# Kernel tuning notes

Measured on AMD Instinct MI355X. Metric: run time of the kernel, lower is better.

The kernel has to match this reference:

```python
import jax, jax.numpy as jnp
import numpy as np

N = 100000      # nodes per node type
E = 500000      # edges per relation
DIN = 128
DOUT = 128
H = 8
DK = DOUT // H  # 16
SQRT_DK = float(np.sqrt(DK))


def setup_inputs() -> dict:
    key = jax.random.key(0)
    ks = jax.random.split(key, 24)
    s = 1.0 / np.sqrt(DIN)
    inp = {
        "h_a": jax.random.normal(ks[0], (N, DIN), jnp.float32),
        "h_b": jax.random.normal(ks[1], (N, DIN), jnp.float32),
        "src0": jax.random.randint(ks[2], (E,), 0, N, jnp.int32),
        "dst0": jax.random.randint(ks[3], (E,), 0, N, jnp.int32),
        "src1": jax.random.randint(ks[4], (E,), 0, N, jnp.int32),
        "dst1": jax.random.randint(ks[5], (E,), 0, N, jnp.int32),
        "src2": jax.random.randint(ks[6], (E,), 0, N, jnp.int32),
        "dst2": jax.random.randint(ks[7], (E,), 0, N, jnp.int32),
        "Wk": jax.random.normal(ks[8], (2, DIN, DOUT), jnp.float32) * s,
        "bk": jnp.zeros((2, DOUT), jnp.float32),
        "Wv": jax.random.normal(ks[9], (2, DIN, DOUT), jnp.float32) * s,
        "bv": jnp.zeros((2, DOUT), jnp.float32),
        "Wq": jax.random.normal(ks[10], (2, DIN, DOUT), jnp.float32) * s,
        "bq": jnp.zeros((2, DOUT), jnp.float32),
        "Wa": jax.random.normal(ks[11], (2, DOUT, DOUT), jnp.float32) * s,
        "ba": jnp.zeros((2, DOUT), jnp.float32),
        # xavier_uniform-like scale for [H, DK, DK] relation transforms
        "rel_att": jax.random.normal(ks[12], (3, H, DK, DK), jnp.float32) * (1.0 / np.sqrt(DK)),
        "rel_msg": jax.random.normal(ks[13], (3, H, DK, DK), jnp.float32) * (1.0 / np.sqrt(DK)),
        "rel_pri": 1.0 + 0.1 * jax.random.normal(ks[14], (3, H), jnp.float32),
        "skip": jnp.zeros((2,), jnp.float32),
    }
    return inp


def _relation(x_src, x_dst, src, dst, Wk_, bk_, Wv_, bv_, Wq_, bq_, att, msg, pri):
    """One canonical edge type: returns scatter-sum aggregation t [N, H, DK]."""
    k = (x_src @ Wk_ + bk_).reshape(-1, H, DK)
    k = jnp.einsum('nhd,hde->nhe', k, att)                     # relation-specific key transform
    v = jnp.einsum('nhd,hde->nhe', (x_src @ Wv_ + bv_).reshape(-1, H, DK), msg)
    q = (x_dst @ Wq_ + bq_).reshape(-1, H, DK)
    # per-edge dot-product score [E, H] (v_dot_u with q on dst, k on src)
    score = jnp.einsum('ehd,ehd->eh', q[dst], k[src]) * pri / SQRT_DK
    # edge softmax grouped by dst node
    smax = jax.ops.segment_max(score, dst, num_segments=N)
    smax = jnp.where(jnp.isfinite(smax), smax, 0.0)            # empty dst groups
    ex = jnp.exp(score - smax[dst])
    den = jax.ops.segment_sum(ex, dst, num_segments=N)
    a = ex / den[dst]                                          # [E, H]
    # message = v[src] * a, scatter-sum to dst
    return jax.ops.segment_sum(v[src] * a[..., None], dst, num_segments=N)


def reference(h_a, h_b, src0, dst0, src1, dst1, src2, dst2,
              Wk, bk, Wv, bv, Wq, bq, Wa, ba,
              rel_att, rel_msg, rel_pri, skip):
    # relations: 0: a->b, 1: b->a, 2: a->b
    t0 = _relation(h_a, h_b, src0, dst0, Wk[0], bk[0], Wv[0], bv[0], Wq[1], bq[1],
                   rel_att[0], rel_msg[0], rel_pri[0])
    t1 = _relation(h_b, h_a, src1, dst1, Wk[1], bk[1], Wv[1], bv[1], Wq[0], bq[0],
                   rel_att[1], rel_msg[1], rel_pri[1])
    t2 = _relation(h_a, h_b, src2, dst2, Wk[0], bk[0], Wv[0], bv[0], Wq[1], bq[1],
                   rel_att[2], rel_msg[2], rel_pri[2])
    t_a = t1.reshape(N, DOUT)                  # cross_reducer mean over 1 relation
    t_b = ((t0 + t2) * 0.5).reshape(N, DOUT)   # mean over 2 relations into type b

    def node_out(t, h, i):
        alpha = jax.nn.sigmoid(skip[i])
        o = t @ Wa[i] + ba[i]                  # dropout = identity (eval)
        return o * alpha + h * (1.0 - alpha)

    out_a = node_out(t_a, h_a, 0)
    out_b = node_out(t_b, h_b, 1)
    return jnp.stack([out_a, out_b])           # [2, N, DOUT]
```

## Files before the change

kernel.cpp:

```cpp
#include <hip/hip_runtime.h>
#include <math.h>

typedef short bf16x8 __attribute__((ext_vector_type(8)));
typedef float f32x4 __attribute__((ext_vector_type(4)));
typedef float f32x2 __attribute__((ext_vector_type(2)));

__device__ __forceinline__ unsigned short cvt_bf16(float f) {
    unsigned u = __float_as_uint(f);
    u += 0x7fffu + ((u >> 16) & 1);
    return (unsigned short)(u >> 16);
}
__device__ __forceinline__ float cvt_f32(unsigned short b) {
    return __uint_as_float(((unsigned)b) << 16);
}
__device__ __forceinline__ f32x2 bf16pair(unsigned u) {
    f32x2 r;
    r.x = __uint_as_float(u << 16);
    r.y = __uint_as_float(u & 0xffff0000u);
    return r;
}

__global__ void compose_kernel(const float* __restrict__ Wk, const float* __restrict__ bk,
                               const float* __restrict__ Wv, const float* __restrict__ bv,
                               const float* __restrict__ att, const float* __restrict__ msg,
                               const float* __restrict__ pri,
                               unsigned short* __restrict__ WkT, unsigned short* __restrict__ WvT,
                               float* __restrict__ bkC, float* __restrict__ bvC) {
    int tid = blockIdx.x * blockDim.x + threadIdx.x;
    if (tid >= 3 * 16384) return;
    int r = tid / 16384;
    int rem = tid & 16383;
    int c = rem >> 7;
    int i = rem & 127;
    int h = c >> 4, e = c & 15;
    int wsel = (r == 1) ? 1 : 0;
    float p = pri[r * 8 + h] * 0.25f;

    const float* wkrow = Wk + wsel * 16384 + i * 128 + h * 16;
    const float* wvrow = Wv + wsel * 16384 + i * 128 + h * 16;
    const float* attc = att + ((r * 8 + h) * 16) * 16 + e;
    const float* msgc = msg + ((r * 8 + h) * 16) * 16 + e;
    float aK = 0.f, aV = 0.f;
#pragma unroll
    for (int d = 0; d < 16; ++d) {
        aK += wkrow[d] * attc[d * 16];
        aV += wvrow[d] * msgc[d * 16];
    }
    WkT[r * 16384 + c * 128 + i] = cvt_bf16(aK * p);
    WvT[r * 16384 + c * 128 + i] = cvt_bf16(aV);
    if (i == 0) {
        const float* bkr = bk + wsel * 128 + h * 16;
        const float* bvr = bv + wsel * 128 + h * 16;
        float bK = 0.f, bV = 0.f;
#pragma unroll
        for (int d = 0; d < 16; ++d) {
            bK += bkr[d] * attc[d * 16];
            bV += bvr[d] * msgc[d * 16];
        }
        bkC[r * 128 + c] = bK * p;
        bvC[r * 128 + c] = bV;
    }
}

__global__ void tcast_kernel(const float* __restrict__ src, unsigned short* __restrict__ dst) {
    int tid = blockIdx.x * 256 + threadIdx.x;
    int c = tid >> 7, i = tid & 127;
    dst[tid] = cvt_bf16(src[i * 128 + c]);
}

__global__ void cast_kernel(const float* __restrict__ src, unsigned short* __restrict__ dst, int n4) {
    int t = blockIdx.x * 256 + threadIdx.x;
    if (t >= n4) return;
    float4 f = ((const float4*)src)[t];
    ushort4 o;
    o.x = cvt_bf16(f.x); o.y = cvt_bf16(f.y); o.z = cvt_bf16(f.z); o.w = cvt_bf16(f.w);
    ((ushort4*)dst)[t] = o;
}

struct OutSpec { const unsigned short* Wt; const float* bias; unsigned short* out; };
struct OutSpecs { OutSpec o[5]; };

#define LPAD 136

__global__ __launch_bounds__(256) void mfma_proj_kernel(const unsigned short* __restrict__ X,
                                                        int nrows, OutSpecs specs, int nout) {
    __shared__ unsigned short Xs[128 * LPAD];
    __shared__ unsigned short Ws[128 * LPAD];
    __shared__ float bs[128];
    int tid = threadIdx.x;
    int n0 = blockIdx.x * 128;
    int rows_in = nrows - n0; if (rows_in > 128) rows_in = 128;

    {
        int rowb = tid >> 4, seg = tid & 15;
#pragma unroll
        for (int p = 0; p < 8; ++p) {
            int row = p * 16 + rowb;
            int rowg = row < rows_in ? row : rows_in - 1;
            uint4 d = *(const uint4*)(X + ((size_t)(n0 + rowg)) * 128 + seg * 8);
            *(uint4*)&Xs[row * LPAD + seg * 8] = d;
        }
    }

    int wave = tid >> 6, lane = tid & 63;
    int l15 = lane & 15, quad = lane >> 4;

    for (int o = 0; o < nout; ++o) {
        {
            int rowb = tid >> 4, seg = tid & 15;
            const unsigned short* Wt = specs.o[o].Wt;
#pragma unroll
            for (int p = 0; p < 8; ++p) {
                int row = p * 16 + rowb;
                uint4 d = *(const uint4*)(Wt + (size_t)row * 128 + seg * 8);
                *(uint4*)&Ws[row * LPAD + seg * 8] = d;
            }
            if (tid < 128) bs[tid] = specs.o[o].bias[tid];
        }
        __syncthreads();

        f32x4 acc[2][8];
#pragma unroll
        for (int mi = 0; mi < 2; ++mi)
#pragma unroll
            for (int nt = 0; nt < 8; ++nt) acc[mi][nt] = (f32x4){0.f, 0.f, 0.f, 0.f};

#pragma unroll
        for (int ks = 0; ks < 4; ++ks) {
            bf16x8 afr[2];
            afr[0] = *(const bf16x8*)&Xs[(wave * 32 + l15) * LPAD + ks * 32 + quad * 8];
            afr[1] = *(const bf16x8*)&Xs[(wave * 32 + 16 + l15) * LPAD + ks * 32 + quad * 8];
#pragma unroll
            for (int nt = 0; nt < 8; ++nt) {
                bf16x8 bfr = *(const bf16x8*)&Ws[(nt * 16 + l15) * LPAD + ks * 32 + quad * 8];
                acc[0][nt] = __builtin_amdgcn_mfma_f32_16x16x32_bf16(afr[0], bfr, acc[0][nt], 0, 0, 0);
                acc[1][nt] = __builtin_amdgcn_mfma_f32_16x16x32_bf16(afr[1], bfr, acc[1][nt], 0, 0, 0);
            }
        }

        unsigned short* out = specs.o[o].out;
#pragma unroll
        for (int mi = 0; mi < 2; ++mi) {
            int rowbase = wave * 32 + mi * 16 + quad * 4;
#pragma unroll
            for (int r = 0; r < 4; ++r) {
                int row = rowbase + r;
                if (row < rows_in) {
#pragma unroll
                    for (int nt = 0; nt < 8; ++nt) {
                        int col = nt * 16 + l15;
                        out[(size_t)(n0 + row) * 128 + col] = cvt_bf16(acc[mi][nt][r] + bs[col]);
                    }
                }
            }
        }
        __syncthreads();
    }
}

__global__ __launch_bounds__(256) void mfma_out_kernel(const unsigned short* __restrict__ T16,
        int nrows, const unsigned short* __restrict__ WaT, const float* __restrict__ bias,
        const float* __restrict__ resid, const float* __restrict__ skipv, int skipidx,
        float* __restrict__ out) {
    __shared__ unsigned short Xs[128 * LPAD];
    __shared__ unsigned short Ws[128 * LPAD];
    __shared__ float bs[128];
    int tid = threadIdx.x;
    int n0 = blockIdx.x * 128;
    int rows_in = nrows - n0; if (rows_in > 128) rows_in = 128;

    {
        int rowb = tid >> 4, seg = tid & 15;
#pragma unroll
        for (int p = 0; p < 8; ++p) {
            int row = p * 16 + rowb;
            int rowg = row < rows_in ? row : rows_in - 1;
            uint4 d = *(const uint4*)(T16 + ((size_t)(n0 + rowg)) * 128 + seg * 8);
            *(uint4*)&Xs[row * LPAD + seg * 8] = d;
            uint4 w = *(const uint4*)(WaT + (size_t)row * 128 + seg * 8);
            *(uint4*)&Ws[row * LPAD + seg * 8] = w;
        }
        if (tid < 128) bs[tid] = bias[tid];
    }
    __syncthreads();

    int wave = tid >> 6, lane = tid & 63;
    int l15 = lane & 15, quad = lane >> 4;

    f32x4 acc[2][8];
#pragma unroll
    for (int mi = 0; mi < 2; ++mi)
#pragma unroll
        for (int nt = 0; nt < 8; ++nt) acc[mi][nt] = (f32x4){0.f, 0.f, 0.f, 0.f};

#pragma unroll
    for (int ks = 0; ks < 4; ++ks) {
        bf16x8 afr[2];
        afr[0] = *(const bf16x8*)&Xs[(wave * 32 + l15) * LPAD + ks * 32 + quad * 8];
        afr[1] = *(const bf16x8*)&Xs[(wave * 32 + 16 + l15) * LPAD + ks * 32 + quad * 8];
#pragma unroll
        for (int nt = 0; nt < 8; ++nt) {
            bf16x8 bfr = *(const bf16x8*)&Ws[(nt * 16 + l15) * LPAD + ks * 32 + quad * 8];
            acc[0][nt] = __builtin_amdgcn_mfma_f32_16x16x32_bf16(afr[0], bfr, acc[0][nt], 0, 0, 0);
            acc[1][nt] = __builtin_amdgcn_mfma_f32_16x16x32_bf16(afr[1], bfr, acc[1][nt], 0, 0, 0);
        }
    }

    float s = skipv[skipidx];
    float alpha = 1.f / (1.f + __expf(-s));
    float beta = 1.f - alpha;
#pragma unroll
    for (int mi = 0; mi < 2; ++mi) {
        int rowbase = wave * 32 + mi * 16 + quad * 4;
#pragma unroll
        for (int r = 0; r < 4; ++r) {
            int row = rowbase + r;
            if (row < rows_in) {
#pragma unroll
                for (int nt = 0; nt < 8; ++nt) {
                    int col = nt * 16 + l15;
                    size_t gi = (size_t)(n0 + row) * 128 + col;
                    out[gi] = alpha * (acc[mi][nt][r] + bs[col]) + beta * resid[gi];
                }
            }
        }
    }
}

__global__ void count_kernel(const int* __restrict__ dst, int* __restrict__ cnt, int E) {
    int e = blockIdx.x * 256 + threadIdx.x;
    if (e < E) atomicAdd(&cnt[dst[e]], 1);
}

#define SCAN_B 256
__global__ void scan1_kernel(const int* __restrict__ cnt, int* __restrict__ offs,
                             int* __restrict__ bsum, int n) {
    __shared__ int sh[SCAN_B];
    int i = blockIdx.x * SCAN_B + threadIdx.x;
    int v = (i < n) ? cnt[i] : 0;
    sh[threadIdx.x] = v;
    __syncthreads();
    for (int off = 1; off < SCAN_B; off <<= 1) {
        int t = (threadIdx.x >= off) ? sh[threadIdx.x - off] : 0;
        __syncthreads();
        sh[threadIdx.x] += t;
        __syncthreads();
    }
    if (i < n) offs[i] = sh[threadIdx.x] - v;
    if (threadIdx.x == SCAN_B - 1) bsum[blockIdx.x] = sh[threadIdx.x];
}

__global__ void scan2_kernel(int* __restrict__ bsum, int nb) {
    __shared__ int sh[512];
    int v = (threadIdx.x < nb) ? bsum[threadIdx.x] : 0;
    sh[threadIdx.x] = v;
    __syncthreads();
    for (int off = 1; off < 512; off <<= 1) {
        int t = (threadIdx.x >= off) ? sh[threadIdx.x - off] : 0;
        __syncthreads();
        sh[threadIdx.x] += t;
        __syncthreads();
    }
    if (threadIdx.x < nb) bsum[threadIdx.x] = sh[threadIdx.x] - v;
}

__global__ void scan3_kernel(int* __restrict__ offs, const int* __restrict__ bsum,
                             int* __restrict__ fill, int n) {
    int i = blockIdx.x * SCAN_B + threadIdx.x;
    if (i < n) {
        int o = offs[i] + bsum[blockIdx.x];
        offs[i] = o;
        fill[i] = o;
    }
}

__global__ void scatter_kernel(const int* __restrict__ src, const int* __restrict__ dst,
                               int* __restrict__ fill, int* __restrict__ ss, int E) {
    int e = blockIdx.x * 256 + threadIdx.x;
    if (e < E) {
        int p = atomicAdd(&fill[dst[e]], 1);
        ss[p] = src[e];
    }
}

__global__ __launch_bounds__(256) void agg_kernel(
    const unsigned short* __restrict__ q, const unsigned short* __restrict__ k,
    const unsigned short* __restrict__ v, const int* __restrict__ offs,
    const int* __restrict__ cnt, const int* __restrict__ ss,
    const float* __restrict__ acc_in, void* __restrict__ outp, int out_bf16,
    float w, int N) {
    int wid = (blockIdx.x * 256 + threadIdx.x) >> 6;
    if (wid >= N) return;
    int lane = threadIdx.x & 63;
    int j = lane >> 3, h = lane & 7;

    const uint4* qp = (const uint4*)(q + (size_t)wid * 128 + h * 16);
    uint4 qa = qp[0], qb = qp[1];
    f32x2 q2[8];
    q2[0] = bf16pair(qa.x); q2[1] = bf16pair(qa.y);
    q2[2] = bf16pair(qa.z); q2[3] = bf16pair(qa.w);
    q2[4] = bf16pair(qb.x); q2[5] = bf16pair(qb.y);
    q2[6] = bf16pair(qb.z); q2[7] = bf16pair(qb.w);

    int start = offs[wid], deg = cnt[wid];
    float den = 0.f;
    f32x2 acc2[8];
#pragma unroll
    for (int t = 0; t < 8; ++t) acc2[t] = (f32x2){0.f, 0.f};

    for (int i = j; i < deg; i += 8) {
        int s = ss[start + i];
        const uint4* kp = (const uint4*)(k + (size_t)s * 128 + h * 16);
        uint4 ka = kp[0], kb = kp[1];
        const uint4* vp = (const uint4*)(v + (size_t)s * 128 + h * 16);
        uint4 va = vp[0], vb = vp[1];

        f32x2 d2 = (f32x2){0.f, 0.f};
        d2 += q2[0] * bf16pair(ka.x);
        d2 += q2[1] * bf16pair(ka.y);
        d2 += q2[2] * bf16pair(ka.z);
        d2 += q2[3] * bf16pair(ka.w);
        d2 += q2[4] * bf16pair(kb.x);
        d2 += q2[5] * bf16pair(kb.y);
        d2 += q2[6] * bf16pair(kb.z);
        d2 += q2[7] * bf16pair(kb.w);
        float sc = d2.x + d2.y;
        float ex = __expf(sc);
        den += ex;
        f32x2 exv = (f32x2){ex, ex};
        acc2[0] += exv * bf16pair(va.x);
        acc2[1] += exv * bf16pair(va.y);
        acc2[2] += exv * bf16pair(va.z);
        acc2[3] += exv * bf16pair(va.w);
        acc2[4] += exv * bf16pair(vb.x);
        acc2[5] += exv * bf16pair(vb.y);
        acc2[6] += exv * bf16pair(vb.z);
        acc2[7] += exv * bf16pair(vb.w);
    }

#pragma unroll
    for (int mask = 8; mask <= 32; mask <<= 1) {
        den += __shfl_xor(den, mask);
#pragma unroll
        for (int t = 0; t < 8; ++t) {
            acc2[t].x += __shfl_xor(acc2[t].x, mask);
            acc2[t].y += __shfl_xor(acc2[t].y, mask);
        }
    }

    if (j == 0) {
        float inv = (deg > 0) ? (w / den) : 0.f;
        size_t base = (size_t)wid * 128 + h * 16;
        float o[16];
#pragma unroll
        for (int t = 0; t < 8; ++t) {
            o[2 * t] = acc2[t].x * inv;
            o[2 * t + 1] = acc2[t].y * inv;
        }
        if (acc_in) {
#pragma unroll
            for (int t = 0; t < 16; ++t) o[t] += acc_in[base + t];
        }
        if (out_bf16) {
            unsigned short* op = (unsigned short*)outp + base;
            ushort4 p0, p1, p2, p3;
            p0.x = cvt_bf16(o[0]);  p0.y = cvt_bf16(o[1]);  p0.z = cvt_bf16(o[2]);  p0.w = cvt_bf16(o[3]);
            p1.x = cvt_bf16(o[4]);  p1.y = cvt_bf16(o[5]);  p1.z = cvt_bf16(o[6]);  p1.w = cvt_bf16(o[7]);
            p2.x = cvt_bf16(o[8]);  p2.y = cvt_bf16(o[9]);  p2.z = cvt_bf16(o[10]); p2.w = cvt_bf16(o[11]);
            p3.x = cvt_bf16(o[12]); p3.y = cvt_bf16(o[13]); p3.z = cvt_bf16(o[14]); p3.w = cvt_bf16(o[15]);
            ((ushort4*)op)[0] = p0; ((ushort4*)op)[1] = p1;
            ((ushort4*)op)[2] = p2; ((ushort4*)op)[3] = p3;
        } else {
            float* op = (float*)outp + base;
#pragma unroll
            for (int t = 0; t < 4; ++t)
                ((float4*)op)[t] = make_float4(o[4 * t], o[4 * t + 1], o[4 * t + 2], o[4 * t + 3]);
        }
    }
}

extern "C" void kernel_launch(void* const* d_in, const int* in_sizes, int n_in,
                              void* d_out, int out_size, void* d_ws, size_t ws_size,
                              hipStream_t stream) {
    const float* h_a = (const float*)d_in[0];
    const float* h_b = (const float*)d_in[1];
    const int* srcs[3] = {(const int*)d_in[2], (const int*)d_in[4], (const int*)d_in[6]};
    const int* dsts[3] = {(const int*)d_in[3], (const int*)d_in[5], (const int*)d_in[7]};
    const float* Wk = (const float*)d_in[8];
    const float* bk = (const float*)d_in[9];
    const float* Wv = (const float*)d_in[10];
    const float* bv = (const float*)d_in[11];
    const float* Wq = (const float*)d_in[12];
    const float* bq = (const float*)d_in[13];
    const float* Wa = (const float*)d_in[14];
    const float* ba = (const float*)d_in[15];
    const float* att = (const float*)d_in[16];
    const float* msg = (const float*)d_in[17];
    const float* pri = (const float*)d_in[18];
    const float* skip = (const float*)d_in[19];

    const int N = in_sizes[0] / 128;
    const int E = in_sizes[2];
    const size_t NC = (size_t)N * 128;

    char* P = (char*)d_ws;
    auto alloc = [&](size_t bytes) { char* p = P; P += (bytes + 255) & ~(size_t)255; return p; };

    unsigned short* WkT = (unsigned short*)alloc(3 * 16384 * 2);
    unsigned short* WvT = (unsigned short*)alloc(3 * 16384 * 2);
    unsigned short* WqT = (unsigned short*)alloc(2 * 16384 * 2);
    unsigned short* WaT = (unsigned short*)alloc(2 * 16384 * 2);
    float* bkC = (float*)alloc(3 * 128 * 4);
    float* bvC = (float*)alloc(3 * 128 * 4);
    unsigned short* Xa16 = (unsigned short*)alloc(NC * 2);
    unsigned short* Xb16 = (unsigned short*)alloc(NC * 2);
    unsigned short* qa16 = (unsigned short*)alloc(NC * 2);
    unsigned short* qb16 = (unsigned short*)alloc(NC * 2);
    unsigned short* k16[3], *v16[3];
    for (int r = 0; r < 3; ++r) {
        k16[r] = (unsigned short*)alloc(NC * 2);
        v16[r] = (unsigned short*)alloc(NC * 2);
    }
    float* t_b = (float*)alloc(NC * 4);
    unsigned short* ta16 = (unsigned short*)alloc(NC * 2);
    unsigned short* tb16 = (unsigned short*)alloc(NC * 2);
    int *cnt[3], *offs[3], *fill[3], *ssb[3];
    for (int r = 0; r < 3; ++r) {
        cnt[r] = (int*)alloc((size_t)N * 4);
        offs[r] = (int*)alloc((size_t)N * 4);
        fill[r] = (int*)alloc((size_t)N * 4);
        ssb[r] = (int*)alloc((size_t)E * 4);
    }
    int* bsum = (int*)alloc(512 * 4);

    int eb = (E + 255) / 256;
    int scanb = (N + SCAN_B - 1) / SCAN_B;

    for (int r = 0; r < 3; ++r) {
        hipMemsetAsync(cnt[r], 0, (size_t)N * sizeof(int), stream);
        count_kernel<<<eb, 256, 0, stream>>>(dsts[r], cnt[r], E);
        scan1_kernel<<<scanb, SCAN_B, 0, stream>>>(cnt[r], offs[r], bsum, N);
        scan2_kernel<<<1, 512, 0, stream>>>(bsum, scanb);
        scan3_kernel<<<scanb, SCAN_B, 0, stream>>>(offs[r], bsum, fill[r], N);
        scatter_kernel<<<eb, 256, 0, stream>>>(srcs[r], dsts[r], fill[r], ssb[r], E);
    }

    compose_kernel<<<(3 * 16384 + 255) / 256, 256, 0, stream>>>(
        Wk, bk, Wv, bv, att, msg, pri, WkT, WvT, bkC, bvC);
    tcast_kernel<<<64, 256, 0, stream>>>(Wq, WqT);
    tcast_kernel<<<64, 256, 0, stream>>>(Wq + 16384, WqT + 16384);
    tcast_kernel<<<64, 256, 0, stream>>>(Wa, WaT);
    tcast_kernel<<<64, 256, 0, stream>>>(Wa + 16384, WaT + 16384);

    int n4 = (int)(NC / 4);
    cast_kernel<<<(n4 + 255) / 256, 256, 0, stream>>>(h_a, Xa16, n4);
    cast_kernel<<<(n4 + 255) / 256, 256, 0, stream>>>(h_b, Xb16, n4);

    int gblocks = (N + 127) / 128;

    OutSpecs sa;
    sa.o[0] = {WqT, bq, qa16};
    sa.o[1] = {WkT + 0 * 16384, bkC + 0 * 128, k16[0]};
    sa.o[2] = {WvT + 0 * 16384, bvC + 0 * 128, v16[0]};
    sa.o[3] = {WkT + 2 * 16384, bkC + 2 * 128, k16[2]};
    sa.o[4] = {WvT + 2 * 16384, bvC + 2 * 128, v16[2]};
    mfma_proj_kernel<<<gblocks, 256, 0, stream>>>(Xa16, N, sa, 5);

    OutSpecs sb;
    sb.o[0] = {WqT + 16384, bq + 128, qb16};
    sb.o[1] = {WkT + 1 * 16384, bkC + 1 * 128, k16[1]};
    sb.o[2] = {WvT + 1 * 16384, bvC + 1 * 128, v16[1]};
    sb.o[3] = {nullptr, nullptr, nullptr};
    sb.o[4] = {nullptr, nullptr, nullptr};
    mfma_proj_kernel<<<gblocks, 256, 0, stream>>>(Xb16, N, sb, 3);

    int ab = (N + 3) / 4;
    agg_kernel<<<ab, 256, 0, stream>>>(qb16, k16[0], v16[0], offs[0], cnt[0], ssb[0],
                                       nullptr, t_b, 0, 0.5f, N);
    agg_kernel<<<ab, 256, 0, stream>>>(qa16, k16[1], v16[1], offs[1], cnt[1], ssb[1],
                                       nullptr, ta16, 1, 1.0f, N);
    agg_kernel<<<ab, 256, 0, stream>>>(qb16, k16[2], v16[2], offs[2], cnt[2], ssb[2],
                                       t_b, tb16, 1, 0.5f, N);

    float* out = (float*)d_out;
    mfma_out_kernel<<<gblocks, 256, 0, stream>>>(ta16, N, WaT, ba, h_a, skip, 0, out);
    mfma_out_kernel<<<gblocks, 256, 0, stream>>>(tb16, N, WaT + 16384, ba + 128, h_b, skip, 1,
                                                 out + NC);
}
```

Baseline: 751.6 us.

## Fuse three relation aggregation kernels into one launch with in-register combine

Replaces three separate edge-aggregation launches with a single kernel whose grid is split in halves: one half processes both a->b relations for each destination node, sharing the q load and combining the two results in registers, and the other half processes the b->a relation. This removes the fp32 t_b intermediate buffer and its write and read-back, drops two kernel launches, and lets the two node types run concurrently on the device. The trade-off is load imbalance, since blocks in the first half do twice the edge work, and higher register pressure from holding two accumulator sets.

```diff
diff --git a/kernel.cpp b/kernel.cpp
--- a/kernel.cpp
+++ b/kernel.cpp
@@ -283,31 +283,16 @@
     }
 }
 
-__global__ __launch_bounds__(256) void agg_kernel(
-    const unsigned short* __restrict__ q, const unsigned short* __restrict__ k,
-    const unsigned short* __restrict__ v, const int* __restrict__ offs,
-    const int* __restrict__ cnt, const int* __restrict__ ss,
-    const float* __restrict__ acc_in, void* __restrict__ outp, int out_bf16,
-    float w, int N) {
-    int wid = (blockIdx.x * 256 + threadIdx.x) >> 6;
-    if (wid >= N) return;
-    int lane = threadIdx.x & 63;
-    int j = lane >> 3, h = lane & 7;
-
-    const uint4* qp = (const uint4*)(q + (size_t)wid * 128 + h * 16);
-    uint4 qa = qp[0], qb = qp[1];
-    f32x2 q2[8];
-    q2[0] = bf16pair(qa.x); q2[1] = bf16pair(qa.y);
-    q2[2] = bf16pair(qa.z); q2[3] = bf16pair(qa.w);
-    q2[4] = bf16pair(qb.x); q2[5] = bf16pair(qb.y);
-    q2[6] = bf16pair(qb.z); q2[7] = bf16pair(qb.w);
-
-    int start = offs[wid], deg = cnt[wid];
-    float den = 0.f;
-    f32x2 acc2[8];
-#pragma unroll
-    for (int t = 0; t < 8; ++t) acc2[t] = (f32x2){0.f, 0.f};
-
+struct AggSt { float den; f32x2 acc[8]; };
+
+__device__ __forceinline__ void agg_loop(const unsigned short* __restrict__ k,
+                                         const unsigned short* __restrict__ v,
+                                         const int* __restrict__ ss,
+                                         int start, int deg, int j, int h,
+                                         const f32x2* q2, AggSt& st) {
+    st.den = 0.f;
+#pragma unroll
+    for (int t = 0; t < 8; ++t) st.acc[t] = (f32x2){0.f, 0.f};
     for (int i = j; i < deg; i += 8) {
         int s = ss[start + i];
         const uint4* kp = (const uint4*)(k + (size_t)s * 128 + h * 16);
@@ -326,55 +311,113 @@
         d2 += q2[7] * bf16pair(kb.w);
         float sc = d2.x + d2.y;
         float ex = __expf(sc);
-        den += ex;
+        st.den += ex;
         f32x2 exv = (f32x2){ex, ex};
-        acc2[0] += exv * bf16pair(va.x);
-        acc2[1] += exv * bf16pair(va.y);
-        acc2[2] += exv * bf16pair(va.z);
-        acc2[3] += exv * bf16pair(va.w);
-        acc2[4] += exv * bf16pair(vb.x);
-        acc2[5] += exv * bf16pair(vb.y);
-        acc2[6] += exv * bf16pair(vb.z);
-        acc2[7] += exv * bf16pair(vb.w);
-    }
-
+        st.acc[0] += exv * bf16pair(va.x);
+        st.acc[1] += exv * bf16pair(va.y);
+        st.acc[2] += exv * bf16pair(va.z);
+        st.acc[3] += exv * bf16pair(va.w);
+        st.acc[4] += exv * bf16pair(vb.x);
+        st.acc[5] += exv * bf16pair(vb.y);
+        st.acc[6] += exv * bf16pair(vb.z);
+        st.acc[7] += exv * bf16pair(vb.w);
+    }
+}
+
+__device__ __forceinline__ void butterfly(AggSt& st) {
 #pragma unroll
     for (int mask = 8; mask <= 32; mask <<= 1) {
-        den += __shfl_xor(den, mask);
+        st.den += __shfl_xor(st.den, mask);
 #pragma unroll
         for (int t = 0; t < 8; ++t) {
-            acc2[t].x += __shfl_xor(acc2[t].x, mask);
-            acc2[t].y += __shfl_xor(acc2[t].y, mask);
-        }
-    }
-
-    if (j == 0) {
-        float inv = (deg > 0) ? (w / den) : 0.f;
-        size_t base = (size_t)wid * 128 + h * 16;
-        float o[16];
-#pragma unroll
-        for (int t = 0; t < 8; ++t) {
-            o[2 * t] = acc2[t].x * inv;
-            o[2 * t + 1] = acc2[t].y * inv;
-        }
-        if (acc_in) {
-#pragma unroll
-            for (int t = 0; t < 16; ++t) o[t] += acc_in[base + t];
-        }
-        if (out_bf16) {
-            unsigned short* op = (unsigned short*)outp + base;
-            ushort4 p0, p1, p2, p3;
-            p0.x = cvt_bf16(o[0]);  p0.y = cvt_bf16(o[1]);  p0.z = cvt_bf16(o[2]);  p0.w = cvt_bf16(o[3]);
-            p1.x = cvt_bf16(o[4]);  p1.y = cvt_bf16(o[5]);  p1.z = cvt_bf16(o[6]);  p1.w = cvt_bf16(o[7]);
-            p2.x = cvt_bf16(o[8]);  p2.y = cvt_bf16(o[9]);  p2.z = cvt_bf16(o[10]); p2.w = cvt_bf16(o[11]);
-            p3.x = cvt_bf16(o[12]); p3.y = cvt_bf16(o[13]); p3.z = cvt_bf16(o[14]); p3.w = cvt_bf16(o[15]);
-            ((ushort4*)op)[0] = p0; ((ushort4*)op)[1] = p1;
-            ((ushort4*)op)[2] = p2; ((ushort4*)op)[3] = p3;
-        } else {
-            float* op = (float*)outp + base;
-#pragma unroll
-            for (int t = 0; t < 4; ++t)
-                ((float4*)op)[t] = make_float4(o[4 * t], o[4 * t + 1], o[4 * t + 2], o[4 * t + 3]);
+            st.acc[t].x += __shfl_xor(st.acc[t].x, mask);
+            st.acc[t].y += __shfl_xor(st.acc[t].y, mask);
+        }
+    }
+}
+
+__device__ __forceinline__ void load_q(const unsigned short* __restrict__ q,
+                                       int wid, int h, f32x2* q2) {
+    const uint4* qp = (const uint4*)(q + (size_t)wid * 128 + h * 16);
+    uint4 qa = qp[0], qb = qp[1];
+    q2[0] = bf16pair(qa.x); q2[1] = bf16pair(qa.y);
+    q2[2] = bf16pair(qa.z); q2[3] = bf16pair(qa.w);
+    q2[4] = bf16pair(qb.x); q2[5] = bf16pair(qb.y);
+    q2[6] = bf16pair(qb.z); q2[7] = bf16pair(qb.w);
+}
+
+__device__ __forceinline__ void store_bf16(unsigned short* __restrict__ outp,
+                                           size_t base, const float* o) {
+    unsigned short* op = outp + base;
+    ushort4 p0, p1, p2, p3;
+    p0.x = cvt_bf16(o[0]);  p0.y = cvt_bf16(o[1]);  p0.z = cvt_bf16(o[2]);  p0.w = cvt_bf16(o[3]);
+    p1.x = cvt_bf16(o[4]);  p1.y = cvt_bf16(o[5]);  p1.z = cvt_bf16(o[6]);  p1.w = cvt_bf16(o[7]);
+    p2.x = cvt_bf16(o[8]);  p2.y = cvt_bf16(o[9]);  p2.z = cvt_bf16(o[10]); p2.w = cvt_bf16(o[11]);
+    p3.x = cvt_bf16(o[12]); p3.y = cvt_bf16(o[13]); p3.z = cvt_bf16(o[14]); p3.w = cvt_bf16(o[15]);
+    ((ushort4*)op)[0] = p0; ((ushort4*)op)[1] = p1;
+    ((ushort4*)op)[2] = p2; ((ushort4*)op)[3] = p3;
+}
+
+__global__ __launch_bounds__(256) void agg_fused_kernel(
+    const unsigned short* __restrict__ qb,
+    const unsigned short* __restrict__ k0, const unsigned short* __restrict__ v0,
+    const int* __restrict__ offs0, const int* __restrict__ cnt0, const int* __restrict__ ss0,
+    const unsigned short* __restrict__ k2, const unsigned short* __restrict__ v2,
+    const int* __restrict__ offs2, const int* __restrict__ cnt2, const int* __restrict__ ss2,
+    const unsigned short* __restrict__ qa,
+    const unsigned short* __restrict__ k1, const unsigned short* __restrict__ v1,
+    const int* __restrict__ offs1, const int* __restrict__ cnt1, const int* __restrict__ ss1,
+    unsigned short* __restrict__ tb16, unsigned short* __restrict__ ta16,
+    int N, int ablk) {
+    int bid = blockIdx.x;
+    int lane = threadIdx.x & 63;
+    int j = lane >> 3, h = lane & 7;
+
+    if (bid < ablk) {
+        int wid = (bid * 256 + (int)threadIdx.x) >> 6;
+        if (wid >= N) return;
+        int start0 = offs0[wid], deg0 = cnt0[wid];
+        int start2 = offs2[wid], deg2 = cnt2[wid];
+        f32x2 q2[8];
+        load_q(qb, wid, h, q2);
+
+        AggSt s0, s2;
+        agg_loop(k0, v0, ss0, start0, deg0, j, h, q2, s0);
+        agg_loop(k2, v2, ss2, start2, deg2, j, h, q2, s2);
+        butterfly(s0);
+        butterfly(s2);
+
+        if (j == 0) {
+            float i0 = (deg0 > 0) ? (0.5f / s0.den) : 0.f;
+            float i2 = (deg2 > 0) ? (0.5f / s2.den) : 0.f;
+            float o[16];
+#pragma unroll
+            for (int t = 0; t < 8; ++t) {
+                o[2 * t]     = s0.acc[t].x * i0 + s2.acc[t].x * i2;
+                o[2 * t + 1] = s0.acc[t].y * i0 + s2.acc[t].y * i2;
+            }
+            store_bf16(tb16, (size_t)wid * 128 + h * 16, o);
+        }
+    } else {
+        int wid = ((bid - ablk) * 256 + (int)threadIdx.x) >> 6;
+        if (wid >= N) return;
+        int start1 = offs1[wid], deg1 = cnt1[wid];
+        f32x2 q2[8];
+        load_q(qa, wid, h, q2);
+
+        AggSt s1;
+        agg_loop(k1, v1, ss1, start1, deg1, j, h, q2, s1);
+        butterfly(s1);
+
+        if (j == 0) {
+            float i1 = (deg1 > 0) ? (1.0f / s1.den) : 0.f;
+            float o[16];
+#pragma unroll
+            for (int t = 0; t < 8; ++t) {
+                o[2 * t]     = s1.acc[t].x * i1;
+                o[2 * t + 1] = s1.acc[t].y * i1;
+            }
+            store_bf16(ta16, (size_t)wid * 128 + h * 16, o);
         }
     }
 }
@@ -421,7 +464,6 @@
         k16[r] = (unsigned short*)alloc(NC * 2);
         v16[r] = (unsigned short*)alloc(NC * 2);
     }
-    float* t_b = (float*)alloc(NC * 4);
     unsigned short* ta16 = (unsigned short*)alloc(NC * 2);
     unsigned short* tb16 = (unsigned short*)alloc(NC * 2);
     int *cnt[3], *offs[3], *fill[3], *ssb[3];
@@ -475,12 +517,11 @@
     mfma_proj_kernel<<<gblocks, 256, 0, stream>>>(Xb16, N, sb, 3);
 
     int ab = (N + 3) / 4;
-    agg_kernel<<<ab, 256, 0, stream>>>(qb16, k16[0], v16[0], offs[0], cnt[0], ssb[0],
-                                       nullptr, t_b, 0, 0.5f, N);
-    agg_kernel<<<ab, 256, 0, stream>>>(qa16, k16[1], v16[1], offs[1], cnt[1], ssb[1],
-                                       nullptr, ta16, 1, 1.0f, N);
-    agg_kernel<<<ab, 256, 0, stream>>>(qb16, k16[2], v16[2], offs[2], cnt[2], ssb[2],
-                                       t_b, tb16, 1, 0.5f, N);
+    agg_fused_kernel<<<2 * ab, 256, 0, stream>>>(
+        qb16, k16[0], v16[0], offs[0], cnt[0], ssb[0],
+        k16[2], v16[2], offs[2], cnt[2], ssb[2],
+        qa16, k16[1], v16[1], offs[1], cnt[1], ssb[1],
+        tb16, ta16, N, ab);
 
     float* out = (float*)d_out;
     mfma_out_kernel<<<gblocks, 256, 0, stream>>>(ta16, N, WaT, ba, h_a, skip, 0, out);
```

After: 724.7 us. -3.6%, faster.
